# Performance work log

Hardware: AMD Instinct MI355X
Metric: run time of the kernel (lower is better)

## Reference

```python
import jax, jax.numpy as jnp
import numpy as np

B, NX, NR, D, H = 8, 512, 512, 256, 256


def setup_inputs() -> dict:
    key = jax.random.key(0)
    ks = jax.random.split(key, 8)
    s = 1.0 / np.sqrt(D)
    sh = 1.0 / np.sqrt(H)
    return {
        "X": jax.random.normal(ks[0], (B, NX, D), dtype=jnp.float32),
        "ref": jax.random.normal(ks[1], (B, NR, D), dtype=jnp.float32),
        "W_X": jax.random.normal(ks[2], (H, D), dtype=jnp.float32) * s,
        "b_X": jax.random.normal(ks[3], (H,), dtype=jnp.float32) * s,
        "W_ref": jax.random.normal(ks[4], (H, D), dtype=jnp.float32) * s,
        "b_ref": jax.random.normal(ks[5], (H,), dtype=jnp.float32) * s,
        "v_w": jax.random.normal(ks[6], (1, H), dtype=jnp.float32) * sh,
        "v_b": jax.random.normal(ks[7], (1,), dtype=jnp.float32) * sh,
    }


def reference(X, ref, W_X, b_X, W_ref, b_ref, v_w, v_b):
    # linear projections: [B, nX, H], [B, nR, H]
    hX = jnp.einsum('bxd,hd->bxh', X, W_X) + b_X
    hR = jnp.einsum('brd,hd->brh', ref, W_ref) + b_ref
    # additive (Bahdanau) scores: [B, nX, nR]
    t = jnp.tanh(hX[:, :, None, :] + hR[:, None, :, :])
    out = jnp.einsum('bxrh,h->bxr', t, v_w[0]) + v_b[0]
    # softmax over the n_X axis (dim=1 in torch)
    attn = jax.nn.softmax(out, axis=1)
    # weighted sum of X per ref position: [B, nR, D]
    weighted_X = jnp.einsum('bxe,bxr->bre', X, attn)
    return weighted_X
```

## Files before the change

### kernel.cpp

```cpp
#include <hip/hip_runtime.h>
#include <math.h>

#define CB 8
#define CNX 512
#define CNR 512
#define CD 256
#define CH 256

typedef __attribute__((ext_vector_type(8))) short short8;
typedef __attribute__((ext_vector_type(4))) float f32x4;

__device__ __forceinline__ float fast_rcp(float x) {
#if __has_builtin(__builtin_amdgcn_rcpf)
  return __builtin_amdgcn_rcpf(x);
#else
  return 1.0f / x;
#endif
}
__device__ __forceinline__ float fast_exp2(float x) {
#if __has_builtin(__builtin_amdgcn_exp2f)
  return __builtin_amdgcn_exp2f(x);
#else
  return exp2f(x);
#endif
}

__device__ __forceinline__ void cvt_store(unsigned short* dstH,
                                          unsigned short* dstL,
                                          float4 v0, float4 v1) {
  unsigned u0x = __float_as_uint(v0.x), u0y = __float_as_uint(v0.y);
  unsigned u0z = __float_as_uint(v0.z), u0w = __float_as_uint(v0.w);
  unsigned u1x = __float_as_uint(v1.x), u1y = __float_as_uint(v1.y);
  unsigned u1z = __float_as_uint(v1.z), u1w = __float_as_uint(v1.w);
  uint4 H;
  H.x = (u0x >> 16) | (u0y & 0xFFFF0000u);
  H.y = (u0z >> 16) | (u0w & 0xFFFF0000u);
  H.z = (u1x >> 16) | (u1y & 0xFFFF0000u);
  H.w = (u1z >> 16) | (u1w & 0xFFFF0000u);
  float r0x = v0.x - __uint_as_float(u0x & 0xFFFF0000u);
  float r0y = v0.y - __uint_as_float(u0y & 0xFFFF0000u);
  float r0z = v0.z - __uint_as_float(u0z & 0xFFFF0000u);
  float r0w = v0.w - __uint_as_float(u0w & 0xFFFF0000u);
  float r1x = v1.x - __uint_as_float(u1x & 0xFFFF0000u);
  float r1y = v1.y - __uint_as_float(u1y & 0xFFFF0000u);
  float r1z = v1.z - __uint_as_float(u1z & 0xFFFF0000u);
  float r1w = v1.w - __uint_as_float(u1w & 0xFFFF0000u);
  uint4 L;
  L.x = (__float_as_uint(r0x) >> 16) | (__float_as_uint(r0y) & 0xFFFF0000u);
  L.y = (__float_as_uint(r0z) >> 16) | (__float_as_uint(r0w) & 0xFFFF0000u);
  L.z = (__float_as_uint(r1x) >> 16) | (__float_as_uint(r1y) & 0xFFFF0000u);
  L.w = (__float_as_uint(r1z) >> 16) | (__float_as_uint(r1w) & 0xFFFF0000u);
  *(uint4*)dstH = H;
  *(uint4*)dstL = L;
}

__global__ __launch_bounds__(256) void proj_mfma(
    const float* __restrict__ A0, const float* __restrict__ A1,
    const float* __restrict__ W0, const float* __restrict__ W1,
    const float* __restrict__ bias0, const float* __restrict__ bias1,
    float* __restrict__ E0, float* __restrict__ E1) {
  __shared__ unsigned short lds[2][4][64][40];
  const int K = CD;
  int z = blockIdx.z;
  const float* A = z ? A1 : A0;
  const float* W = z ? W1 : W0;
  const float* bias = z ? bias1 : bias0;
  float* ET = z ? E1 : E0;
  int m0 = blockIdx.x * 64, n0 = blockIdx.y * 64;
  int tid = threadIdx.x;
  int lane = tid & 63, w = tid >> 6;
  int wm = w >> 1, wn = w & 1;
  int r = tid >> 2, kq = (tid & 3) * 8;
  const float* pA = A + (size_t)(m0 + r) * K + kq;
  const float* pW = W + (size_t)(n0 + r) * K + kq;
  f32x4 acc[2][2] = {};
  float4 a0 = *(const float4*)(pA);
  float4 a1 = *(const float4*)(pA + 4);
  float4 w0 = *(const float4*)(pW);
  float4 w1 = *(const float4*)(pW + 4);
  cvt_store(&lds[0][0][r][kq], &lds[0][1][r][kq], a0, a1);
  cvt_store(&lds[0][2][r][kq], &lds[0][3][r][kq], w0, w1);
  for (int s = 0; s < 8; s++) {
    __syncthreads();
    if (s < 7) {
      int kt = (s + 1) * 32;
      a0 = *(const float4*)(pA + kt);
      a1 = *(const float4*)(pA + kt + 4);
      w0 = *(const float4*)(pW + kt);
      w1 = *(const float4*)(pW + kt + 4);
    }
    int cur = s & 1;
    int arow = wm * 32 + (lane & 15);
    int brow = wn * 32 + (lane & 15);
    int koff = (lane >> 4) * 8;
    short8 ah0 = *(const short8*)&lds[cur][0][arow][koff];
    short8 ah1 = *(const short8*)&lds[cur][0][arow + 16][koff];
    short8 al0 = *(const short8*)&lds[cur][1][arow][koff];
    short8 al1 = *(const short8*)&lds[cur][1][arow + 16][koff];
    short8 bh0 = *(const short8*)&lds[cur][2][brow][koff];
    short8 bh1 = *(const short8*)&lds[cur][2][brow + 16][koff];
    short8 bl0 = *(const short8*)&lds[cur][3][brow][koff];
    short8 bl1 = *(const short8*)&lds[cur][3][brow + 16][koff];
    acc[0][0] = __builtin_amdgcn_mfma_f32_16x16x32_bf16(ah0, bh0, acc[0][0], 0, 0, 0);
    acc[0][1] = __builtin_amdgcn_mfma_f32_16x16x32_bf16(ah0, bh1, acc[0][1], 0, 0, 0);
    acc[1][0] = __builtin_amdgcn_mfma_f32_16x16x32_bf16(ah1, bh0, acc[1][0], 0, 0, 0);
    acc[1][1] = __builtin_amdgcn_mfma_f32_16x16x32_bf16(ah1, bh1, acc[1][1], 0, 0, 0);
    acc[0][0] = __builtin_amdgcn_mfma_f32_16x16x32_bf16(ah0, bl0, acc[0][0], 0, 0, 0);
    acc[0][1] = __builtin_amdgcn_mfma_f32_16x16x32_bf16(ah0, bl1, acc[0][1], 0, 0, 0);
    acc[1][0] = __builtin_amdgcn_mfma_f32_16x16x32_bf16(ah1, bl0, acc[1][0], 0, 0, 0);
    acc[1][1] = __builtin_amdgcn_mfma_f32_16x16x32_bf16(ah1, bl1, acc[1][1], 0, 0, 0);
    acc[0][0] = __builtin_amdgcn_mfma_f32_16x16x32_bf16(al0, bh0, acc[0][0], 0, 0, 0);
    acc[0][1] = __builtin_amdgcn_mfma_f32_16x16x32_bf16(al0, bh1, acc[0][1], 0, 0, 0);
    acc[1][0] = __builtin_amdgcn_mfma_f32_16x16x32_bf16(al1, bh0, acc[1][0], 0, 0, 0);
    acc[1][1] = __builtin_amdgcn_mfma_f32_16x16x32_bf16(al1, bh1, acc[1][1], 0, 0, 0);
    if (s < 7) {
      int nxt = cur ^ 1;
      cvt_store(&lds[nxt][0][r][kq], &lds[nxt][1][r][kq], a0, a1);
      cvt_store(&lds[nxt][2][r][kq], &lds[nxt][3][r][kq], w0, w1);
    }
  }
  const float K2L = 2.8853900817779268f;
  int b = m0 >> 9;
  int xq = (m0 & 511) + wm * 32 + (lane >> 4) * 4;
#pragma unroll
  for (int mi = 0; mi < 2; mi++) {
#pragma unroll
    for (int ni = 0; ni < 2; ni++) {
      int h = n0 + wn * 32 + ni * 16 + (lane & 15);
      float bb = bias[h];
      f32x4 a = acc[mi][ni];
      float4 o = {fast_exp2(K2L * (a[0] + bb)), fast_exp2(K2L * (a[1] + bb)),
                  fast_exp2(K2L * (a[2] + bb)), fast_exp2(K2L * (a[3] + bb))};
      *(float4*)(ET + ((size_t)b * CH + h) * CNX + xq + mi * 16) = o;
    }
  }
}

__global__ __launch_bounds__(512) void scores_kernel(
    const float* __restrict__ exT, const float* __restrict__ erT,
    const float* __restrict__ v_w, float* __restrict__ scT) {
  __shared__ float smem[4 * 2048 + 256];
  int b = blockIdx.z;
  int x0 = blockIdx.x * 64, r0 = blockIdx.y * 64;
  int tid = threadIdx.x;
  int g = tid >> 8;
  int t = tid & 255;
  float* xs = smem + g * 4096;
  float* rs = xs + 2048;
  float* vsh = smem + 8192;
  if (tid < 256) vsh[tid] = v_w[tid];
  int tx = t & 15, ty = t >> 4;
  int sr = t >> 4, sc = (t & 15) * 4;
  int wrot = (tid >> 6) & 7;
  const float* pX = exT + (size_t)b * CH * CNX + x0 + sc;
  const float* pR = erT + (size_t)b * CH * CNR + r0 + sc;
  int hb = g * 32;
  float4 xa0 = *(const float4*)(pX + (size_t)(hb + sr) * CNX);
  float4 xa1 = *(const float4*)(pX + (size_t)(hb + sr + 16) * CNX);
  float4 ra0 = *(const float4*)(pR + (size_t)(hb + sr) * CNR);
  float4 ra1 = *(const float4*)(pR + (size_t)(hb + sr + 16) * CNR);
  float acc[4][4] = {};
  for (int hc = hb; hc < CH; hc += 64) {
    __syncthreads();
    *(float4*)&xs[sr * 64 + sc] = xa0;
    *(float4*)&xs[(sr + 16) * 64 + sc] = xa1;
    *(float4*)&rs[sr * 64 + sc] = ra0;
    *(float4*)&rs[(sr + 16) * 64 + sc] = ra1;
    __syncthreads();
    if (hc + 64 < CH) {
      xa0 = *(const float4*)(pX + (size_t)(hc + 64 + sr) * CNX);
      xa1 = *(const float4*)(pX + (size_t)(hc + 64 + sr + 16) * CNX);
      ra0 = *(const float4*)(pR + (size_t)(hc + 64 + sr) * CNR);
      ra1 = *(const float4*)(pR + (size_t)(hc + 64 + sr + 16) * CNR);
    }
#pragma unroll 2
    for (int hq = 0; hq < 8; hq++) {
      int h0 = ((hq + wrot) & 7) * 4;
      float4 vv = *(const float4*)&vsh[hc + h0];
      float4 xv0 = *(const float4*)&xs[(h0 + 0) * 64 + tx * 4];
      float4 xv1 = *(const float4*)&xs[(h0 + 1) * 64 + tx * 4];
      float4 xv2 = *(const float4*)&xs[(h0 + 2) * 64 + tx * 4];
      float4 xv3 = *(const float4*)&xs[(h0 + 3) * 64 + tx * 4];
      float4 rv0 = *(const float4*)&rs[(h0 + 0) * 64 + ty * 4];
      float4 rv1 = *(const float4*)&rs[(h0 + 1) * 64 + ty * 4];
      float4 rv2 = *(const float4*)&rs[(h0 + 2) * 64 + ty * 4];
      float4 rv3 = *(const float4*)&rs[(h0 + 3) * 64 + ty * 4];
      float xm0[4] = {xv0.x, xv0.y, xv0.z, xv0.w};
      float xm1[4] = {xv1.x, xv1.y, xv1.z, xv1.w};
      float xm2[4] = {xv2.x, xv2.y, xv2.z, xv2.w};
      float xm3[4] = {xv3.x, xv3.y, xv3.z, xv3.w};
      float rm0[4] = {rv0.x, rv0.y, rv0.z, rv0.w};
      float rm1[4] = {rv1.x, rv1.y, rv1.z, rv1.w};
      float rm2[4] = {rv2.x, rv2.y, rv2.z, rv2.w};
      float rm3[4] = {rv3.x, rv3.y, rv3.z, rv3.w};
#pragma unroll
      for (int i = 0; i < 4; i++)
#pragma unroll
        for (int j = 0; j < 4; j++) {
          float a = fmaf(rm0[i], xm0[j], 1.0f);
          float bb = fmaf(rm1[i], xm1[j], 1.0f);
          float c = fmaf(rm2[i], xm2[j], 1.0f);
          float d = fmaf(rm3[i], xm3[j], 1.0f);
          float q12 = a * bb, q34 = c * d;
          float p12 = fmaf(vv.y, a, vv.x * bb);
          float p34 = fmaf(vv.w, c, vv.z * d);
          float num = fmaf(p34, q12, p12 * q34);
          acc[i][j] = fmaf(num, fast_rcp(q12 * q34), acc[i][j]);
        }
    }
  }
  __syncthreads();
  float* mg = smem;
  if (g == 1) {
#pragma unroll
    for (int i = 0; i < 4; i++)
#pragma unroll
      for (int j = 0; j < 4; j++)
        mg[t + 256 * (i * 4 + j)] = acc[i][j];
  }
  __syncthreads();
  if (g == 0) {
    float* pO = scT + ((size_t)b * CNR + r0 + ty * 4) * CNX + x0 + tx * 4;
#pragma unroll
    for (int i = 0; i < 4; i++) {
      float4 o = {-2.0f * (acc[i][0] + mg[t + 256 * (i * 4 + 0)]),
                  -2.0f * (acc[i][1] + mg[t + 256 * (i * 4 + 1)]),
                  -2.0f * (acc[i][2] + mg[t + 256 * (i * 4 + 2)]),
                  -2.0f * (acc[i][3] + mg[t + 256 * (i * 4 + 3)])};
      *(float4*)(pO + (size_t)i * CNX) = o;
    }
  }
}

__global__ __launch_bounds__(512) void wsum_fused(
    const float* __restrict__ scT, const float* __restrict__ X,
    float* __restrict__ out) {
  __shared__ float smem[4 * 2176 + 128];
  const float L2E = 1.4426950408889634f;
  int b = blockIdx.z;
  int r0 = blockIdx.x * 64, d0 = blockIdx.y * 64;
  int tid = threadIdx.x;
  int g = tid >> 8;
  int t = tid & 255;
  float* As = smem + g * 4352;
  float* Bs = As + 2176;
  float* dnn = smem + 8704;
  int tx = t & 15, ty = t >> 4;
  int ar = t >> 2, ak = (t & 3) * 4;
  int br = t >> 4, bc = (t & 15) * 4;
  int krot = ((tid >> 6) & 7) * 4;
  int kb = g * 32;
  const float* pS = scT + ((size_t)b * CNR + r0 + ar) * CNX + ak;
  const float* pB = X + (size_t)b * CNX * CD + d0 + bc;
  float acc[4][4] = {};
  float dsum = 0.0f;
  float4 s0 = *(const float4*)(pS + kb);
  float4 s1 = *(const float4*)(pS + kb + 16);
  float4 b0 = *(const float4*)(pB + (size_t)(kb + br) * CD);
  float4 b1 = *(const float4*)(pB + (size_t)(kb + br + 16) * CD);
  for (int kt = kb; kt < CNX; kt += 64) {
    float4 e0 = {fast_exp2(s0.x * L2E), fast_exp2(s0.y * L2E),
                 fast_exp2(s0.z * L2E), fast_exp2(s0.w * L2E)};
    float4 e1 = {fast_exp2(s1.x * L2E), fast_exp2(s1.y * L2E),
                 fast_exp2(s1.z * L2E), fast_exp2(s1.w * L2E)};
    dsum += ((e0.x + e0.y) + (e0.z + e0.w)) + ((e1.x + e1.y) + (e1.z + e1.w));
    __syncthreads();
    As[(ak + 0) * 68 + ar] = e0.x;
    As[(ak + 1) * 68 + ar] = e0.y;
    As[(ak + 2) * 68 + ar] = e0.z;
    As[(ak + 3) * 68 + ar] = e0.w;
    As[(ak + 16) * 68 + ar] = e1.x;
    As[(ak + 17) * 68 + ar] = e1.y;
    As[(ak + 18) * 68 + ar] = e1.z;
    As[(ak + 19) * 68 + ar] = e1.w;
    *(float4*)&Bs[br * 68 + bc] = b0;
    *(float4*)&Bs[(br + 16) * 68 + bc] = b1;
    __syncthreads();
    if (kt + 64 < CNX) {
      s0 = *(const float4*)(pS + kt + 64);
      s1 = *(const float4*)(pS + kt + 80);
      b0 = *(const float4*)(pB + (size_t)(kt + 64 + br) * CD);
      b1 = *(const float4*)(pB + (size_t)(kt + 64 + br + 16) * CD);
    }
#pragma unroll 8
    for (int k = 0; k < 32; k++) {
      int kk = (k + krot) & 31;
      float4 a4 = *(const float4*)&As[kk * 68 + ty * 4];
      float4 b4 = *(const float4*)&Bs[kk * 68 + tx * 4];
      float am[4] = {a4.x, a4.y, a4.z, a4.w};
      float bm[4] = {b4.x, b4.y, b4.z, b4.w};
#pragma unroll
      for (int i = 0; i < 4; i++)
#pragma unroll
        for (int j = 0; j < 4; j++)
          acc[i][j] = fmaf(am[i], bm[j], acc[i][j]);
    }
  }
  dsum += __shfl_xor(dsum, 1, 64);
  dsum += __shfl_xor(dsum, 2, 64);
  if ((t & 3) == 0) dnn[g * 64 + ar] = dsum;
  __syncthreads();
  float* mg = smem;
  if (g == 1) {
#pragma unroll
    for (int i = 0; i < 4; i++)
#pragma unroll
      for (int j = 0; j < 4; j++)
        mg[t + 256 * (i * 4 + j)] = acc[i][j];
  }
  __syncthreads();
  if (g == 0) {
    float invm[4];
#pragma unroll
    for (int i = 0; i < 4; i++)
      invm[i] = fast_rcp(dnn[ty * 4 + i] + dnn[64 + ty * 4 + i]);
    float* pO = out + ((size_t)b * CNR + r0 + ty * 4) * CD + d0 + tx * 4;
#pragma unroll
    for (int i = 0; i < 4; i++) {
      float4 o = {
          (acc[i][0] + mg[t + 256 * (i * 4 + 0)]) * invm[i],
          (acc[i][1] + mg[t + 256 * (i * 4 + 1)]) * invm[i],
          (acc[i][2] + mg[t + 256 * (i * 4 + 2)]) * invm[i],
          (acc[i][3] + mg[t + 256 * (i * 4 + 3)]) * invm[i]};
      *(float4*)(pO + (size_t)i * CD) = o;
    }
  }
}

extern "C" void kernel_launch(void* const* d_in, const int* in_sizes, int n_in,
                              void* d_out, int out_size, void* d_ws, size_t ws_size,
                              hipStream_t stream) {
  const float* X     = (const float*)d_in[0];
  const float* ref   = (const float*)d_in[1];
  const float* W_X   = (const float*)d_in[2];
  const float* b_X   = (const float*)d_in[3];
  const float* W_ref = (const float*)d_in[4];
  const float* b_ref = (const float*)d_in[5];
  const float* v_w   = (const float*)d_in[6];
  float* out = (float*)d_out;
  float* ws  = (float*)d_ws;

  float* exT = ws;
  float* erT = ws + 1048576;
  float* scT = ws + 2097152;

  proj_mfma<<<dim3(64, 4, 2), 256, 0, stream>>>(X, ref, W_X, W_ref, b_X, b_ref, exT, erT);
  scores_kernel<<<dim3(8, 8, 8), 512, 0, stream>>>(exT, erT, v_w, scT);
  wsum_fused<<<dim3(8, 4, 8), 512, 0, stream>>>(scT, X, out);
}
```

Baseline: 146.3 us.

## Port weighted-sum GEMM to bf16x3 split MFMA with double-buffered swizzled LDS

Replaces the scalar-FMA fp32 weighted-sum kernel with one that splits the softmax numerators and X values into bf16 high/low parts. It accumulates three bf16 MFMA products per tile to approximate fp32 precision. Tiles are double-buffered in XOR-swizzled LDS, and the next tile's global loads overlap the current MFMAs. The goal is to cut the FMA-bound cost of the final GEMM, at the price of split overhead and slightly lower precision than full fp32.

```diff
diff --git a/kernel.cpp b/kernel.cpp
--- a/kernel.cpp
+++ b/kernel.cpp
@@ -52,6 +52,23 @@
   L.w = (__float_as_uint(r1z) >> 16) | (__float_as_uint(r1w) & 0xFFFF0000u);
   *(uint4*)dstH = H;
   *(uint4*)dstL = L;
+}
+
+__device__ __forceinline__ void split4(float4 v, ushort4* H, ushort4* L) {
+  unsigned ux = __float_as_uint(v.x), uy = __float_as_uint(v.y);
+  unsigned uz = __float_as_uint(v.z), uw = __float_as_uint(v.w);
+  H->x = (unsigned short)(ux >> 16);
+  H->y = (unsigned short)(uy >> 16);
+  H->z = (unsigned short)(uz >> 16);
+  H->w = (unsigned short)(uw >> 16);
+  float rx = v.x - __uint_as_float(ux & 0xFFFF0000u);
+  float ry = v.y - __uint_as_float(uy & 0xFFFF0000u);
+  float rz = v.z - __uint_as_float(uz & 0xFFFF0000u);
+  float rw = v.w - __uint_as_float(uw & 0xFFFF0000u);
+  L->x = (unsigned short)(__float_as_uint(rx) >> 16);
+  L->y = (unsigned short)(__float_as_uint(ry) >> 16);
+  L->z = (unsigned short)(__float_as_uint(rz) >> 16);
+  L->w = (unsigned short)(__float_as_uint(rw) >> 16);
 }
 
 __global__ __launch_bounds__(256) void proj_mfma(
@@ -232,98 +249,102 @@
   }
 }
 
-__global__ __launch_bounds__(512) void wsum_fused(
+__global__ __launch_bounds__(512) void wsum_mfma(
     const float* __restrict__ scT, const float* __restrict__ X,
     float* __restrict__ out) {
-  __shared__ float smem[4 * 2176 + 128];
+  __shared__ unsigned short lds[2][2][64][64];
+  __shared__ float dn[64];
   const float L2E = 1.4426950408889634f;
   int b = blockIdx.z;
   int r0 = blockIdx.x * 64, d0 = blockIdx.y * 64;
   int tid = threadIdx.x;
-  int g = tid >> 8;
-  int t = tid & 255;
-  float* As = smem + g * 4352;
-  float* Bs = As + 2176;
-  float* dnn = smem + 8704;
-  int tx = t & 15, ty = t >> 4;
-  int ar = t >> 2, ak = (t & 3) * 4;
-  int br = t >> 4, bc = (t & 15) * 4;
-  int krot = ((tid >> 6) & 7) * 4;
-  int kb = g * 32;
-  const float* pS = scT + ((size_t)b * CNR + r0 + ar) * CNX + ak;
-  const float* pB = X + (size_t)b * CNX * CD + d0 + bc;
-  float acc[4][4] = {};
+  int lane = tid & 63, w = tid >> 6;
+  int wm = w >> 2, wn = w & 3;
+  int pr = tid >> 3, pxk = (tid & 7) * 4;
+  int psl = pxk >> 3, pof = pxk & 7;
+  int xd = tid & 63, xx = (tid >> 6) * 4;
+  int xsl = xx >> 3, xof = xx & 7;
+  const float* pS = scT + ((size_t)b * CNR + r0 + pr) * CNX + pxk;
+  const float* pX = X + ((size_t)b * CNX + xx) * CD + d0 + xd;
+  f32x4 acc0 = {}, acc1 = {};
   float dsum = 0.0f;
-  float4 s0 = *(const float4*)(pS + kb);
-  float4 s1 = *(const float4*)(pS + kb + 16);
-  float4 b0 = *(const float4*)(pB + (size_t)(kb + br) * CD);
-  float4 b1 = *(const float4*)(pB + (size_t)(kb + br + 16) * CD);
-  for (int kt = kb; kt < CNX; kt += 64) {
-    float4 e0 = {fast_exp2(s0.x * L2E), fast_exp2(s0.y * L2E),
-                 fast_exp2(s0.z * L2E), fast_exp2(s0.w * L2E)};
-    float4 e1 = {fast_exp2(s1.x * L2E), fast_exp2(s1.y * L2E),
-                 fast_exp2(s1.z * L2E), fast_exp2(s1.w * L2E)};
-    dsum += ((e0.x + e0.y) + (e0.z + e0.w)) + ((e1.x + e1.y) + (e1.z + e1.w));
+  float4 sv = *(const float4*)(pS);
+  float4 xv = {pX[0], pX[CD], pX[2 * CD], pX[3 * CD]};
+  {
+    float4 ev = {fast_exp2(sv.x * L2E), fast_exp2(sv.y * L2E),
+                 fast_exp2(sv.z * L2E), fast_exp2(sv.w * L2E)};
+    dsum += (ev.x + ev.y) + (ev.z + ev.w);
+    ushort4 H, L;
+    split4(ev, &H, &L);
+    unsigned short* rp = &lds[0][0][pr][0];
+    *(ushort4*)(rp + ((psl ^ (pr & 7)) << 3) + pof) = H;
+    *(ushort4*)(rp + (((psl + 4) ^ (pr & 7)) << 3) + pof) = L;
+    split4(xv, &H, &L);
+    unsigned short* rx = &lds[0][1][xd][0];
+    *(ushort4*)(rx + ((xsl ^ (xd & 7)) << 3) + xof) = H;
+    *(ushort4*)(rx + (((xsl + 4) ^ (xd & 7)) << 3) + xof) = L;
+  }
+  int q = lane >> 4;
+  int mr0 = wm * 32 + (lane & 15);
+  int mr1 = mr0 + 16;
+  int nr = wn * 16 + (lane & 15);
+  for (int s = 0; s < 16; s++) {
     __syncthreads();
-    As[(ak + 0) * 68 + ar] = e0.x;
-    As[(ak + 1) * 68 + ar] = e0.y;
-    As[(ak + 2) * 68 + ar] = e0.z;
-    As[(ak + 3) * 68 + ar] = e0.w;
-    As[(ak + 16) * 68 + ar] = e1.x;
-    As[(ak + 17) * 68 + ar] = e1.y;
-    As[(ak + 18) * 68 + ar] = e1.z;
-    As[(ak + 19) * 68 + ar] = e1.w;
-    *(float4*)&Bs[br * 68 + bc] = b0;
-    *(float4*)&Bs[(br + 16) * 68 + bc] = b1;
-    __syncthreads();
-    if (kt + 64 < CNX) {
-      s0 = *(const float4*)(pS + kt + 64);
-      s1 = *(const float4*)(pS + kt + 80);
-      b0 = *(const float4*)(pB + (size_t)(kt + 64 + br) * CD);
-      b1 = *(const float4*)(pB + (size_t)(kt + 64 + br + 16) * CD);
-    }
-#pragma unroll 8
-    for (int k = 0; k < 32; k++) {
-      int kk = (k + krot) & 31;
-      float4 a4 = *(const float4*)&As[kk * 68 + ty * 4];
-      float4 b4 = *(const float4*)&Bs[kk * 68 + tx * 4];
-      float am[4] = {a4.x, a4.y, a4.z, a4.w};
-      float bm[4] = {b4.x, b4.y, b4.z, b4.w};
-#pragma unroll
-      for (int i = 0; i < 4; i++)
-#pragma unroll
-        for (int j = 0; j < 4; j++)
-          acc[i][j] = fmaf(am[i], bm[j], acc[i][j]);
+    if (s < 15) {
+      int kt = (s + 1) * 32;
+      sv = *(const float4*)(pS + kt);
+      xv.x = pX[(size_t)(kt + 0) * CD];
+      xv.y = pX[(size_t)(kt + 1) * CD];
+      xv.z = pX[(size_t)(kt + 2) * CD];
+      xv.w = pX[(size_t)(kt + 3) * CD];
+    }
+    int cur = s & 1;
+    const unsigned short* Pt = &lds[cur][0][0][0];
+    const unsigned short* Xt = &lds[cur][1][0][0];
+    short8 ah0 = *(const short8*)(Pt + mr0 * 64 + ((q ^ (mr0 & 7)) << 3));
+    short8 al0 = *(const short8*)(Pt + mr0 * 64 + (((q + 4) ^ (mr0 & 7)) << 3));
+    short8 ah1 = *(const short8*)(Pt + mr1 * 64 + ((q ^ (mr1 & 7)) << 3));
+    short8 al1 = *(const short8*)(Pt + mr1 * 64 + (((q + 4) ^ (mr1 & 7)) << 3));
+    short8 bh = *(const short8*)(Xt + nr * 64 + ((q ^ (nr & 7)) << 3));
+    short8 bl = *(const short8*)(Xt + nr * 64 + (((q + 4) ^ (nr & 7)) << 3));
+    acc0 = __builtin_amdgcn_mfma_f32_16x16x32_bf16(ah0, bh, acc0, 0, 0, 0);
+    acc1 = __builtin_amdgcn_mfma_f32_16x16x32_bf16(ah1, bh, acc1, 0, 0, 0);
+    acc0 = __builtin_amdgcn_mfma_f32_16x16x32_bf16(ah0, bl, acc0, 0, 0, 0);
+    acc1 = __builtin_amdgcn_mfma_f32_16x16x32_bf16(ah1, bl, acc1, 0, 0, 0);
+    acc0 = __builtin_amdgcn_mfma_f32_16x16x32_bf16(al0, bh, acc0, 0, 0, 0);
+    acc1 = __builtin_amdgcn_mfma_f32_16x16x32_bf16(al1, bh, acc1, 0, 0, 0);
+    if (s < 15) {
+      int nxt = cur ^ 1;
+      float4 ev = {fast_exp2(sv.x * L2E), fast_exp2(sv.y * L2E),
+                   fast_exp2(sv.z * L2E), fast_exp2(sv.w * L2E)};
+      dsum += (ev.x + ev.y) + (ev.z + ev.w);
+      ushort4 H, L;
+      split4(ev, &H, &L);
+      unsigned short* rp = &lds[nxt][0][pr][0];
+      *(ushort4*)(rp + ((psl ^ (pr & 7)) << 3) + pof) = H;
+      *(ushort4*)(rp + (((psl + 4) ^ (pr & 7)) << 3) + pof) = L;
+      split4(xv, &H, &L);
+      unsigned short* rx = &lds[nxt][1][xd][0];
+      *(ushort4*)(rx + ((xsl ^ (xd & 7)) << 3) + xof) = H;
+      *(ushort4*)(rx + (((xsl + 4) ^ (xd & 7)) << 3) + xof) = L;
     }
   }
   dsum += __shfl_xor(dsum, 1, 64);
   dsum += __shfl_xor(dsum, 2, 64);
-  if ((t & 3) == 0) dnn[g * 64 + ar] = dsum;
+  dsum += __shfl_xor(dsum, 4, 64);
+  if ((tid & 7) == 0) dn[pr] = dsum;
   __syncthreads();
-  float* mg = smem;
-  if (g == 1) {
-#pragma unroll
-    for (int i = 0; i < 4; i++)
-#pragma unroll
-      for (int j = 0; j < 4; j++)
-        mg[t + 256 * (i * 4 + j)] = acc[i][j];
-  }
-  __syncthreads();
-  if (g == 0) {
-    float invm[4];
-#pragma unroll
-    for (int i = 0; i < 4; i++)
-      invm[i] = fast_rcp(dnn[ty * 4 + i] + dnn[64 + ty * 4 + i]);
-    float* pO = out + ((size_t)b * CNR + r0 + ty * 4) * CD + d0 + tx * 4;
-#pragma unroll
-    for (int i = 0; i < 4; i++) {
-      float4 o = {
-          (acc[i][0] + mg[t + 256 * (i * 4 + 0)]) * invm[i],
-          (acc[i][1] + mg[t + 256 * (i * 4 + 1)]) * invm[i],
-          (acc[i][2] + mg[t + 256 * (i * 4 + 2)]) * invm[i],
-          (acc[i][3] + mg[t + 256 * (i * 4 + 3)]) * invm[i]};
-      *(float4*)(pO + (size_t)i * CD) = o;
-    }
+  int col = d0 + wn * 16 + (lane & 15);
+  float* pO = out + ((size_t)b * CNR + r0) * CD + col;
+#pragma unroll
+  for (int j = 0; j < 4; j++) {
+    int row = wm * 32 + q * 4 + j;
+    pO[(size_t)row * CD] = acc0[j] * fast_rcp(dn[row]);
+  }
+#pragma unroll
+  for (int j = 0; j < 4; j++) {
+    int row = wm * 32 + 16 + q * 4 + j;
+    pO[(size_t)row * CD] = acc1[j] * fast_rcp(dn[row]);
   }
 }
 
@@ -346,5 +367,5 @@
 
   proj_mfma<<<dim3(64, 4, 2), 256, 0, stream>>>(X, ref, W_X, W_ref, b_X, b_ref, exT, erT);
   scores_kernel<<<dim3(8, 8, 8), 512, 0, stream>>>(exT, erT, v_w, scT);
-  wsum_fused<<<dim3(8, 4, 8), 512, 0, stream>>>(scT, X, out);
-}
+  wsum_mfma<<<dim3(8, 4, 8), 512, 0, stream>>>(scT, X, out);
+}
```

New measurement: 132.8 us. 9.2% less time.
